# Kernel optimization log

Measured on AMD Instinct MI355X. Metric: run time of the kernel, lower is better.

## Reference

```python
import jax, jax.numpy as jnp
import numpy as np

N_BUS = 200000; N_GEN = 50000
E_BB = 1600000; E_GB = 400000; E_BG = 400000
D_IN = 64; H = 32
OUT_BUS = 4; OUT_GEN = 2


def setup_inputs() -> dict:
    key = jax.random.key(0)
    it = iter(jax.random.split(key, 48))
    def nrm(shape, s=0.05):
        return jax.random.normal(next(it), shape, jnp.float32) * s
    inp = {}
    inp["x_bus"] = jax.random.normal(next(it), (N_BUS, D_IN), jnp.float32)
    inp["x_gen"] = jax.random.normal(next(it), (N_GEN, D_IN), jnp.float32)
    inp["src_bb"] = jax.random.randint(next(it), (E_BB,), 0, N_BUS)
    inp["dst_bb"] = jax.random.randint(next(it), (E_BB,), 0, N_BUS)
    inp["src_gb"] = jax.random.randint(next(it), (E_GB,), 0, N_GEN)
    inp["dst_gb"] = jax.random.randint(next(it), (E_GB,), 0, N_BUS)
    inp["src_bg"] = jax.random.randint(next(it), (E_BG,), 0, N_BUS)
    inp["dst_bg"] = jax.random.randint(next(it), (E_BG,), 0, N_GEN)
    # SAGEConv params per layer / relation: lin_l (on aggregated neighbors, with bias),
    # lin_r (root weight on x_dst, no bias) -- matches PyG SAGEConv defaults.
    for lname, din in (("l1", D_IN), ("l2", H)):
        for rel in ("bb", "gb", "bg"):
            inp[f"{lname}_{rel}_Wl"] = nrm((din, H))
            inp[f"{lname}_{rel}_bl"] = jnp.zeros((H,), jnp.float32)
            inp[f"{lname}_{rel}_Wr"] = nrm((din, H))
    for nt, dout in (("bus", OUT_BUS), ("gen", OUT_GEN)):
        inp[f"lin0_{nt}_W"] = nrm((H, H))
        inp[f"lin0_{nt}_b"] = jnp.zeros((H,), jnp.float32)
        inp[f"linf_{nt}_W"] = nrm((H, dout))
        inp[f"linf_{nt}_b"] = jnp.zeros((dout,), jnp.float32)
    return inp


def _sage(x_src, x_dst, src, dst, Wl, bl, Wr, n_dst):
    # SAGEConv: mean-aggregate neighbor features, then out = lin_l(mean) + lin_r(x_dst)
    msg = jax.ops.segment_sum(x_src[src], dst, num_segments=n_dst)
    cnt = jax.ops.segment_sum(jnp.ones((src.shape[0],), x_src.dtype), dst, num_segments=n_dst)
    mean = msg / jnp.maximum(cnt, 1.0)[:, None]
    return mean @ Wl + bl + x_dst @ Wr


def reference(x_bus, x_gen, src_bb, dst_bb, src_gb, dst_gb, src_bg, dst_bg,
              l1_bb_Wl, l1_bb_bl, l1_bb_Wr, l1_gb_Wl, l1_gb_bl, l1_gb_Wr,
              l1_bg_Wl, l1_bg_bl, l1_bg_Wr,
              l2_bb_Wl, l2_bb_bl, l2_bb_Wr, l2_gb_Wl, l2_gb_bl, l2_gb_Wr,
              l2_bg_Wl, l2_bg_bl, l2_bg_Wr,
              lin0_bus_W, lin0_bus_b, lin0_gen_W, lin0_gen_b,
              linf_bus_W, linf_bus_b, linf_gen_W, linf_gen_b):
    # HeteroConv layer 1 (aggr='sum' over relations targeting each dst type)
    hb = (_sage(x_bus, x_bus, src_bb, dst_bb, l1_bb_Wl, l1_bb_bl, l1_bb_Wr, N_BUS)
          + _sage(x_gen, x_bus, src_gb, dst_gb, l1_gb_Wl, l1_gb_bl, l1_gb_Wr, N_BUS))
    hg = _sage(x_bus, x_gen, src_bg, dst_bg, l1_bg_Wl, l1_bg_bl, l1_bg_Wr, N_GEN)
    xb, xg = jax.nn.relu(hb), jax.nn.relu(hg)  # dropout is identity in eval mode
    # HeteroConv layer 2
    hb = (_sage(xb, xb, src_bb, dst_bb, l2_bb_Wl, l2_bb_bl, l2_bb_Wr, N_BUS)
          + _sage(xg, xb, src_gb, dst_gb, l2_gb_Wl, l2_gb_bl, l2_gb_Wr, N_BUS))
    hg = _sage(xb, xg, src_bg, dst_bg, l2_bg_Wl, l2_bg_bl, l2_bg_Wr, N_GEN)
    xb, xg = jax.nn.relu(hb), jax.nn.relu(hg)
    # per-node-type hidden Linear (input relu'd again as in the original; relu is idempotent)
    xb = jax.nn.relu(xb) @ lin0_bus_W + lin0_bus_b
    xg = jax.nn.relu(xg) @ lin0_gen_W + lin0_gen_b
    out_bus = xb @ linf_bus_W + linf_bus_b
    out_gen = xg @ linf_gen_W + linf_gen_b
    return out_bus, out_gen
```

## Files before the change

kernel.cpp:

```cpp
#include <hip/hip_runtime.h>
#include <hip/hip_bf16.h>

#define N_BUS 200000
#define N_GEN 50000
#define E_BB 1600000
#define E_GB 400000
#define E_BG 400000
#define H 32
#define NBINS 1024
#define EPT 16

#define NBK_BUS 782
#define NBK_GEN 196
#define CAP_BB 2560
#define CAP_GB 768
#define CAP_BG 2560

#define NB_PART_BB 391
#define NB_PART_GB 98
#define NB_PART_BG 98
#define NB_PART_ALL 587
#define NB_PREP 32
#define NB_TF_BUS 782
#define NB_TF_GEN 196
#define NB_TF_ALL 978
#define NB_FINE_ALL 1760
#define NB_PL_BUS 6250
#define NB_PL_GEN 1563

#define PNONE 0xFFFFFFFFu

typedef __attribute__((ext_vector_type(8))) short short8;
typedef __attribute__((ext_vector_type(4))) float floatx4;

__device__ inline unsigned short f2bf(float f) {
    __hip_bfloat16 h = __float2bfloat16(f);
    return *reinterpret_cast<unsigned short*>(&h);
}
__device__ inline float bf2f(unsigned short u) {
    return __uint_as_float(((unsigned)u) << 16);
}

__global__ __launch_bounds__(256) void zero_kernel(unsigned* __restrict__ p) {
    int i = blockIdx.x * 256 + threadIdx.x;
    if (i < 3 * NBINS) p[i] = 0u;
}

__device__ __forceinline__ void part_body(int blk, const int* __restrict__ src,
                                          const int* __restrict__ dst, int nE,
                                          unsigned* __restrict__ cnt_g, int CAP,
                                          unsigned* __restrict__ pairs) {
    __shared__ unsigned hist[NBINS];
    __shared__ unsigned base[NBINS];
    __shared__ unsigned sbase[NBINS];
    __shared__ unsigned sh[256];
    __shared__ unsigned pairv[256 * EPT];
    __shared__ unsigned short bid[256 * EPT];
    const int tid = threadIdx.x;
    const int cbase = blk * (256 * EPT);
    const int total = min(256 * EPT, nE - cbase);

    unsigned es[EPT], ed[EPT];
#pragma unroll
    for (int q = 0; q < EPT; q++) {
        int i = cbase + q * 256 + tid;
        if (i < nE) { es[q] = (unsigned)src[i]; ed[q] = (unsigned)dst[i]; }
        else ed[q] = PNONE;
    }
    for (int i = tid; i < NBINS; i += 256) hist[i] = 0;
    __syncthreads();
#pragma unroll
    for (int q = 0; q < EPT; q++)
        if (ed[q] != PNONE) atomicAdd(&hist[ed[q] >> 8], 1u);
    __syncthreads();

    unsigned h4[4];
    unsigned s = 0;
#pragma unroll
    for (int k2 = 0; k2 < 4; k2++) { h4[k2] = hist[tid * 4 + k2]; s += h4[k2]; }
    sh[tid] = s;
    __syncthreads();
#pragma unroll
    for (int d = 1; d < 256; d <<= 1) {
        unsigned t = (tid >= d) ? sh[tid - d] : 0u;
        __syncthreads();
        sh[tid] += t;
        __syncthreads();
    }
    unsigned run = sh[tid] - s;
#pragma unroll
    for (int k2 = 0; k2 < 4; k2++) {
        int b = tid * 4 + k2;
        sbase[b] = run;
        base[b] = h4[k2] ? ((unsigned)b * CAP + atomicAdd(&cnt_g[b], h4[k2])) : 0u;
        hist[b] = 0;
        run += h4[k2];
    }
    __syncthreads();

#pragma unroll
    for (int q = 0; q < EPT; q++) {
        if (ed[q] != PNONE) {
            unsigned b = ed[q] >> 8;
            unsigned off = atomicAdd(&hist[b], 1u);
            unsigned p = sbase[b] + off;
            pairv[p] = ((ed[q] & 255u) << 24) | es[q];
            bid[p] = (unsigned short)b;
        }
    }
    __syncthreads();

    for (int p = tid; p < total; p += 256) {
        unsigned b = bid[p];
        pairs[base[b] + ((unsigned)p - sbase[b])] = pairv[p];
    }
}

__device__ __forceinline__ void prep_body(int pb,
    const float* __restrict__ l1_bb_Wl, const float* __restrict__ l1_bb_bl, const float* __restrict__ l1_bb_Wr,
    const float* __restrict__ l1_gb_Wl, const float* __restrict__ l1_gb_bl, const float* __restrict__ l1_gb_Wr,
    const float* __restrict__ l1_bg_Wl, const float* __restrict__ l1_bg_bl, const float* __restrict__ l1_bg_Wr,
    const float* __restrict__ l2_bb_Wl, const float* __restrict__ l2_bb_bl, const float* __restrict__ l2_bb_Wr,
    const float* __restrict__ l2_gb_Wl, const float* __restrict__ l2_gb_bl, const float* __restrict__ l2_gb_Wr,
    const float* __restrict__ l2_bg_Wl, const float* __restrict__ l2_bg_bl, const float* __restrict__ l2_bg_Wr,
    const float* __restrict__ lin0_bus_W, const float* __restrict__ lin0_bus_b,
    const float* __restrict__ linf_bus_W, const float* __restrict__ linf_bus_b,
    const float* __restrict__ lin0_gen_W, const float* __restrict__ lin0_gen_b,
    const float* __restrict__ linf_gen_W, const float* __restrict__ linf_gen_b,
    unsigned short* __restrict__ Wf1b, float* __restrict__ B1b,
    unsigned short* __restrict__ Wf1g, float* __restrict__ B1g,
    unsigned short* __restrict__ Wf2b, float* __restrict__ B2b,
    unsigned short* __restrict__ Wf2g, float* __restrict__ B2g,
    float* __restrict__ WeB, float* __restrict__ beB,
    float* __restrict__ WeG, float* __restrict__ beG)
{
    int t0 = pb * 256 + threadIdx.x;
    const int NT = NB_PREP * 256;

    for (int f = t0; f < 2 * 6 * 64 * 8; f += NT) {
        int j = f & 7, l = (f >> 3) & 63, tile = f >> 9;
        int nt = tile % 6, kt = tile / 6;
        int k = kt * 32 + (l >> 4) * 8 + j, n = nt * 16 + (l & 15);
        float v;
        if (n < 32) v = l1_bb_Wl[k * 32 + n];
        else if (n < 64) v = l1_bg_Wl[k * 32 + n - 32];
        else v = l1_bb_Wr[k * 32 + n - 64] + l1_gb_Wr[k * 32 + n - 64];
        Wf1b[f] = f2bf(v);
    }
    for (int f = t0; f < 2 * 4 * 64 * 8; f += NT) {
        int j = f & 7, l = (f >> 3) & 63, tile = f >> 9;
        int nt = tile % 4, kt = tile / 4;
        int k = kt * 32 + (l >> 4) * 8 + j, n = nt * 16 + (l & 15);
        float v = (n < 32) ? l1_gb_Wl[k * 32 + n] : l1_bg_Wr[k * 32 + n - 32];
        Wf1g[f] = f2bf(v);
    }
    for (int f = t0; f < 6 * 64 * 8; f += NT) {
        int j = f & 7, l = (f >> 3) & 63, nt = f >> 9;
        int k = (l >> 4) * 8 + j, n = nt * 16 + (l & 15);
        float v;
        if (n < 32) v = l2_bb_Wl[k * 32 + n];
        else if (n < 64) v = l2_bg_Wl[k * 32 + n - 32];
        else v = l2_bb_Wr[k * 32 + n - 64] + l2_gb_Wr[k * 32 + n - 64];
        Wf2b[f] = f2bf(v);
    }
    for (int f = t0; f < 4 * 64 * 8; f += NT) {
        int j = f & 7, l = (f >> 3) & 63, nt = f >> 9;
        int k = (l >> 4) * 8 + j, n = nt * 16 + (l & 15);
        float v = (n < 32) ? l2_gb_Wl[k * 32 + n] : l2_bg_Wr[k * 32 + n - 32];
        Wf2g[f] = f2bf(v);
    }
    if (t0 < 96) {
        B1b[t0] = (t0 < 64) ? 0.0f : l1_bb_bl[t0 - 64] + l1_gb_bl[t0 - 64];
        B2b[t0] = (t0 < 64) ? 0.0f : l2_bb_bl[t0 - 64] + l2_gb_bl[t0 - 64];
    }
    if (t0 < 64) {
        B1g[t0] = (t0 < 32) ? 0.0f : l1_bg_bl[t0 - 32];
        B2g[t0] = (t0 < 32) ? 0.0f : l2_bg_bl[t0 - 32];
    }
    if (t0 < 128) {
        int k = t0 >> 2, c = t0 & 3;
        float s = 0.0f;
        for (int m = 0; m < 32; m++) s += lin0_bus_W[k * 32 + m] * linf_bus_W[m * 4 + c];
        WeB[t0] = s;
    }
    if (t0 >= 128 && t0 < 132) {
        int c = t0 - 128;
        float s = linf_bus_b[c];
        for (int m = 0; m < 32; m++) s += lin0_bus_b[m] * linf_bus_W[m * 4 + c];
        beB[c] = s;
    }
    if (t0 >= 132 && t0 < 196) {
        int i = t0 - 132, k = i >> 1, c = i & 1;
        float s = 0.0f;
        for (int m = 0; m < 32; m++) s += lin0_gen_W[k * 32 + m] * linf_gen_W[m * 2 + c];
        WeG[i] = s;
    }
    if (t0 >= 196 && t0 < 198) {
        int c = t0 - 196;
        float s = linf_gen_b[c];
        for (int m = 0; m < 32; m++) s += lin0_gen_b[m] * linf_gen_W[m * 2 + c];
        beG[c] = s;
    }
}

__global__ __launch_bounds__(256) void prep_part_kernel(
    const int* __restrict__ sbb, const int* __restrict__ dbb, unsigned* __restrict__ cbb, unsigned* __restrict__ pbb,
    const int* __restrict__ sgb, const int* __restrict__ dgb, unsigned* __restrict__ cgb, unsigned* __restrict__ pgb,
    const int* __restrict__ sbg, const int* __restrict__ dbg, unsigned* __restrict__ cbg, unsigned* __restrict__ pbg,
    const float* __restrict__ l1_bb_Wl, const float* __restrict__ l1_bb_bl, const float* __restrict__ l1_bb_Wr,
    const float* __restrict__ l1_gb_Wl, const float* __restrict__ l1_gb_bl, const float* __restrict__ l1_gb_Wr,
    const float* __restrict__ l1_bg_Wl, const float* __restrict__ l1_bg_bl, const float* __restrict__ l1_bg_Wr,
    const float* __restrict__ l2_bb_Wl, const float* __restrict__ l2_bb_bl, const float* __restrict__ l2_bb_Wr,
    const float* __restrict__ l2_gb_Wl, const float* __restrict__ l2_gb_bl, const float* __restrict__ l2_gb_Wr,
    const float* __restrict__ l2_bg_Wl, const float* __restrict__ l2_bg_bl, const float* __restrict__ l2_bg_Wr,
    const float* __restrict__ lin0_bus_W, const float* __restrict__ lin0_bus_b,
    const float* __restrict__ linf_bus_W, const float* __restrict__ linf_bus_b,
    const float* __restrict__ lin0_gen_W, const float* __restrict__ lin0_gen_b,
    const float* __restrict__ linf_gen_W, const float* __restrict__ linf_gen_b,
    unsigned short* __restrict__ Wf1b, float* __restrict__ B1b,
    unsigned short* __restrict__ Wf1g, float* __restrict__ B1g,
    unsigned short* __restrict__ Wf2b, float* __restrict__ B2b,
    unsigned short* __restrict__ Wf2g, float* __restrict__ B2g,
    float* __restrict__ WeB, float* __restrict__ beB,
    float* __restrict__ WeG, float* __restrict__ beG)
{
    int b = blockIdx.x;
    if (b < NB_PART_BB) part_body(b, sbb, dbb, E_BB, cbb, CAP_BB, pbb);
    else if (b < NB_PART_BB + NB_PART_GB) part_body(b - NB_PART_BB, sgb, dgb, E_GB, cgb, CAP_GB, pgb);
    else if (b < NB_PART_ALL) part_body(b - NB_PART_BB - NB_PART_GB, sbg, dbg, E_BG, cbg, CAP_BG, pbg);
    else prep_body(b - NB_PART_ALL,
                   l1_bb_Wl, l1_bb_bl, l1_bb_Wr, l1_gb_Wl, l1_gb_bl, l1_gb_Wr,
                   l1_bg_Wl, l1_bg_bl, l1_bg_Wr, l2_bb_Wl, l2_bb_bl, l2_bb_Wr,
                   l2_gb_Wl, l2_gb_bl, l2_gb_Wr, l2_bg_Wl, l2_bg_bl, l2_bg_Wr,
                   lin0_bus_W, lin0_bus_b, linf_bus_W, linf_bus_b,
                   lin0_gen_W, lin0_gen_b, linf_gen_W, linf_gen_b,
                   Wf1b, B1b, Wf1g, B1g, Wf2b, B2b, Wf2g, B2g, WeB, beB, WeG, beG);
}

__device__ __forceinline__ void fine_body(int b, const unsigned* __restrict__ cnt_g, int CAP,
                                          const unsigned* __restrict__ pairs,
                                          unsigned* __restrict__ rs,
                                          unsigned* __restrict__ esrc, int nDst,
                                          char* __restrict__ lds) {
    unsigned* cnt = (unsigned*)lds;
    unsigned* sh = (unsigned*)(lds + 1024);
    unsigned* stg = (unsigned*)(lds + 2048);
    const int tid = threadIdx.x;
    const unsigned start = (unsigned)b * CAP;
    const unsigned m = cnt_g[b];
    const unsigned end = start + m;

    cnt[tid] = 0;
    __syncthreads();
    for (unsigned k = start + tid; k < end; k += 256)
        atomicAdd(&cnt[pairs[k] >> 24], 1u);
    __syncthreads();
    unsigned c = cnt[tid];
    sh[tid] = c;
    __syncthreads();
#pragma unroll
    for (int d = 1; d < 256; d <<= 1) {
        unsigned t = (tid >= d) ? sh[tid - d] : 0u;
        __syncthreads();
        sh[tid] += t;
        __syncthreads();
    }
    int gd = b * 256 + tid;
    unsigned rowstart = start + sh[tid] - c;
    if (gd < nDst) rs[gd] = (rowstart << 9) | (c < 511u ? c : 511u);
    cnt[tid] = sh[tid] - c;
    __syncthreads();
    for (unsigned k = start + tid; k < end; k += 256) {
        unsigned p = pairs[k];
        unsigned off = atomicAdd(&cnt[p >> 24], 1u);
        stg[off] = p & 0x00FFFFFFu;
    }
    __syncthreads();
    for (unsigned p = tid; p < m; p += 256) esrc[start + p] = stg[p];
}

template <int K, int NOUT, int XS>
__device__ __forceinline__ void mfma_tail(
    int rows, int base,
    const unsigned short* __restrict__ Wf, const float* __restrict__ bias,
    unsigned short* __restrict__ y0, unsigned short* __restrict__ y1, float* __restrict__ h,
    short* lx, float* lo)
{
    constexpr int KT = K / 32, NTN = NOUT / 16, NCH = NOUT / 32;
    constexpr int OS = 34;
    const int tid = threadIdx.x;
    const int w = tid >> 6, l = tid & 63, quad = l >> 4, ln = l & 15;

    short8 bf[KT][NTN];
    const short8* wf8 = (const short8*)Wf;
#pragma unroll
    for (int kt = 0; kt < KT; kt++)
#pragma unroll
        for (int nt = 0; nt < NTN; nt++)
            bf[kt][nt] = wf8[(kt * NTN + nt) * 64 + l];
    float bv[NTN];
#pragma unroll
    for (int nt = 0; nt < NTN; nt++) bv[nt] = bias[nt * 16 + ln];

    floatx4 acc[4][NTN];
#pragma unroll
    for (int mt = 0; mt < 4; mt++)
#pragma unroll
        for (int nt = 0; nt < NTN; nt++) {
            floatx4 c0 = {bv[nt], bv[nt], bv[nt], bv[nt]};
            acc[mt][nt] = c0;
        }
#pragma unroll
    for (int mt = 0; mt < 4; mt++) {
        const int row = w * 64 + mt * 16 + ln;
#pragma unroll
        for (int kt = 0; kt < KT; kt++) {
            short8 af = *(const short8*)&lx[row * XS + kt * 32 + quad * 8];
#pragma unroll
            for (int nt = 0; nt < NTN; nt++)
                acc[mt][nt] = __builtin_amdgcn_mfma_f32_16x16x32_bf16(
                    af, bf[kt][nt], acc[mt][nt], 0, 0, 0);
        }
    }

#pragma unroll
    for (int c = 0; c < NCH; c++) {
        __syncthreads();
#pragma unroll
        for (int mt = 0; mt < 4; mt++)
#pragma unroll
            for (int d = 0; d < 2; d++) {
                int nt = 2 * c + d;
#pragma unroll
                for (int r = 0; r < 4; r++)
                    lo[(w * 64 + mt * 16 + quad * 4 + r) * OS + d * 16 + ln] = acc[mt][nt][r];
            }
        __syncthreads();
        const int T4 = rows * 8;
        if (c == NCH - 1) {
            float* og = h + (size_t)base * 32;
            for (int q = tid; q < T4; q += 256) {
                int r = q >> 3, cc = (q & 7) * 4;
                const float* p = &lo[r * OS + cc];
                *(float4*)(og + q * 4) = make_float4(p[0], p[1], p[2], p[3]);
            }
        } else {
            unsigned short* og = ((c == 0) ? y0 : y1) + (size_t)base * 32;
            for (int q = tid; q < T4; q += 256) {
                int r = q >> 3, cc = (q & 7) * 4;
                const float* p = &lo[r * OS + cc];
                short4 s4;
                s4.x = (short)f2bf(p[0]); s4.y = (short)f2bf(p[1]);
                s4.z = (short)f2bf(p[2]); s4.w = (short)f2bf(p[3]);
                *(short4*)(og + q * 4) = s4;
            }
        }
    }
}

template <int K, int NOUT>
__device__ __forceinline__ void transform_body(
    int blk, const float* x, int n,
    const unsigned short* __restrict__ Wf, const float* __restrict__ bias,
    unsigned short* __restrict__ y0, unsigned short* __restrict__ y1, float* h,
    char* ldsraw)
{
    constexpr int XS = K + 8;
    short* lx = (short*)ldsraw;
    const int tid = threadIdx.x;
    const int base = blk * 256;
    const int rows = min(256, n - base);

    {
        const float4* xg = (const float4*)(x + (size_t)base * K);
        const int T4 = rows * (K / 4);
        for (int q = tid; q < T4; q += 256) {
            float4 v = xg[q];
            int r = q / (K / 4), c = (q % (K / 4)) * 4;
            short4 s4;
            s4.x = (short)f2bf(v.x); s4.y = (short)f2bf(v.y);
            s4.z = (short)f2bf(v.z); s4.w = (short)f2bf(v.w);
            *(short4*)&lx[r * XS + c] = s4;
        }
    }
    __syncthreads();
    mfma_tail<K, NOUT, XS>(rows, base, Wf, bias, y0, y1, h, (short*)ldsraw, (float*)ldsraw);
}

__global__ __launch_bounds__(256) void tf1_fine_kernel(
    const float* xb, const unsigned short* __restrict__ Wfb, const float* __restrict__ Bb,
    unsigned short* __restrict__ yb0, unsigned short* __restrict__ yb1, float* hb,
    const float* xg, const unsigned short* __restrict__ Wfg, const float* __restrict__ Bg,
    unsigned short* __restrict__ yg0, float* hg,
    const unsigned* __restrict__ cbb, const unsigned* __restrict__ pbb, unsigned* __restrict__ rsbb, unsigned* __restrict__ ebb,
    const unsigned* __restrict__ cgb, const unsigned* __restrict__ pgb, unsigned* __restrict__ rsgb, unsigned* __restrict__ egb,
    const unsigned* __restrict__ cbg, const unsigned* __restrict__ pbg, unsigned* __restrict__ rsbg, unsigned* __restrict__ ebg)
{
    constexpr int XB = 256 * (64 + 8) * 2, OB = 256 * 34 * 4;
    __shared__ __align__(16) char ldsraw[(XB > OB) ? XB : OB];
    int b = blockIdx.x;
    if (b < NB_TF_BUS)
        transform_body<64, 96>(b, xb, N_BUS, Wfb, Bb, yb0, yb1, hb, ldsraw);
    else if (b < NB_TF_ALL)
        transform_body<64, 64>(b - NB_TF_BUS, xg, N_GEN, Wfg, Bg, yg0, nullptr, hg, ldsraw);
    else {
        int f = b - NB_TF_ALL;
        if (f < NBK_BUS) fine_body(f, cbb, CAP_BB, pbb, rsbb, ebb, N_BUS, ldsraw);
        else if (f < 2 * NBK_BUS) fine_body(f - NBK_BUS, cgb, CAP_GB, pgb, rsgb, egb, N_BUS, ldsraw);
        else fine_body(f - 2 * NBK_BUS, cbg, CAP_BG, pbg, rsbg, ebg, N_GEN, ldsraw);
    }
}

__device__ __forceinline__ void agg_one(
    unsigned u, const unsigned* __restrict__ e,
    const unsigned short* __restrict__ y, int j, float4& r)
{
    unsigned k0 = u >> 9;
    unsigned c = u & 511u;
    unsigned k1 = k0 + c;
    float4 a0 = make_float4(0.f, 0.f, 0.f, 0.f);
    float4 a1 = a0, a2 = a0, a3 = a0;
    unsigned k = k0;
    if (k + 4 <= k1) {
        unsigned s0 = e[k], s1 = e[k + 1], s2 = e[k + 2], s3 = e[k + 3];
        for (; k + 8 <= k1; k += 4) {
            unsigned t0 = e[k + 4], t1 = e[k + 5], t2 = e[k + 6], t3 = e[k + 7];
            ushort4 v0 = *(const ushort4*)(y + (size_t)s0 * H + j);
            ushort4 v1 = *(const ushort4*)(y + (size_t)s1 * H + j);
            ushort4 v2 = *(const ushort4*)(y + (size_t)s2 * H + j);
            ushort4 v3 = *(const ushort4*)(y + (size_t)s3 * H + j);
            a0.x += bf2f(v0.x); a0.y += bf2f(v0.y); a0.z += bf2f(v0.z); a0.w += bf2f(v0.w);
            a1.x += bf2f(v1.x); a1.y += bf2f(v1.y); a1.z += bf2f(v1.z); a1.w += bf2f(v1.w);
            a2.x += bf2f(v2.x); a2.y += bf2f(v2.y); a2.z += bf2f(v2.z); a2.w += bf2f(v2.w);
            a3.x += bf2f(v3.x); a3.y += bf2f(v3.y); a3.z += bf2f(v3.z); a3.w += bf2f(v3.w);
            s0 = t0; s1 = t1; s2 = t2; s3 = t3;
        }
        {
            ushort4 v0 = *(const ushort4*)(y + (size_t)s0 * H + j);
            ushort4 v1 = *(const ushort4*)(y + (size_t)s1 * H + j);
            ushort4 v2 = *(const ushort4*)(y + (size_t)s2 * H + j);
            ushort4 v3 = *(const ushort4*)(y + (size_t)s3 * H + j);
            a0.x += bf2f(v0.x); a0.y += bf2f(v0.y); a0.z += bf2f(v0.z); a0.w += bf2f(v0.w);
            a1.x += bf2f(v1.x); a1.y += bf2f(v1.y); a1.z += bf2f(v1.z); a1.w += bf2f(v1.w);
            a2.x += bf2f(v2.x); a2.y += bf2f(v2.y); a2.z += bf2f(v2.z); a2.w += bf2f(v2.w);
            a3.x += bf2f(v3.x); a3.y += bf2f(v3.y); a3.z += bf2f(v3.z); a3.w += bf2f(v3.w);
            k += 4;
        }
    }
    for (; k < k1; ++k) {
        unsigned s = e[k];
        const ushort4 v = *(const ushort4*)(y + (size_t)s * H + j);
        a0.x += bf2f(v.x); a0.y += bf2f(v.y); a0.z += bf2f(v.z); a0.w += bf2f(v.w);
    }
    a0.x += a1.x + a2.x + a3.x; a0.y += a1.y + a2.y + a3.y;
    a0.z += a1.z + a2.z + a3.z; a0.w += a1.w + a2.w + a3.w;
    float inv = 1.0f / (float)(c > 1u ? c : 1u);
    r.x += a0.x * inv; r.y += a0.y * inv; r.z += a0.z * inv; r.w += a0.w * inv;
}

template <int NTA, bool HASB>
__device__ __forceinline__ void pull_tf_body(
    int blk, int n,
    const unsigned* __restrict__ rsA, const unsigned* __restrict__ eA, const unsigned short* __restrict__ yA,
    const unsigned* __restrict__ rsB, const unsigned* __restrict__ eB, const unsigned short* __restrict__ yB,
    float* __restrict__ h,
    const unsigned short* __restrict__ Wf, const float* __restrict__ bias,
    unsigned short* __restrict__ z0, unsigned short* __restrict__ z1,
    short* __restrict__ lx, float* __restrict__ lo)
{
    constexpr int XS = 40;
    constexpr int OS = 34;
    const int tid = threadIdx.x;
    const int row = tid >> 3;
    const int j = (tid & 7) * 4;
    const int base = blk * 32;
    const int node = base + row;
    const bool act = node < n;

    float4 r = make_float4(0.f, 0.f, 0.f, 0.f);
    if (act) {
        r = *(const float4*)(h + (size_t)node * H + j);
        agg_one(rsA[node], eA, yA, j, r);
        if (HASB) agg_one(rsB[node], eB, yB, j, r);
    }
    short4 s4;
    s4.x = (short)f2bf(fmaxf(r.x, 0.f));
    s4.y = (short)f2bf(fmaxf(r.y, 0.f));
    s4.z = (short)f2bf(fmaxf(r.z, 0.f));
    s4.w = (short)f2bf(fmaxf(r.w, 0.f));
    *(short4*)&lx[row * XS + j] = s4;
    __syncthreads();

    const int w = tid >> 6, l = tid & 63, quad = l >> 4, ln = l & 15;
    const int mt = w & 1, ngrp = w >> 1;
    const short8* wf8 = (const short8*)Wf;
    floatx4 acc[NTA];
    short8 af = *(const short8*)&lx[(mt * 16 + ln) * XS + quad * 8];
#pragma unroll
    for (int i = 0; i < NTA; i++) {
        int nt = 2 * i + ngrp;
        float bv = bias[nt * 16 + ln];
        floatx4 c0 = {bv, bv, bv, bv};
        acc[i] = __builtin_amdgcn_mfma_f32_16x16x32_bf16(af, wf8[nt * 64 + l], c0, 0, 0, 0);
    }

    const int rows = min(32, n - base);
    const int orow = tid >> 3, oc = (tid & 7) * 4;
#pragma unroll
    for (int c = 0; c < NTA; c++) {
        __syncthreads();
#pragma unroll
        for (int rr = 0; rr < 4; rr++)
            lo[(mt * 16 + quad * 4 + rr) * OS + ngrp * 16 + ln] = acc[c][rr];
        __syncthreads();
        if (orow < rows) {
            const float* p = &lo[orow * OS + oc];
            if (c == NTA - 1) {
                *(float4*)(h + (size_t)(base + orow) * H + oc) =
                    make_float4(p[0], p[1], p[2], p[3]);
            } else {
                unsigned short* og = (c == 0) ? z0 : z1;
                short4 o;
                o.x = (short)f2bf(p[0]); o.y = (short)f2bf(p[1]);
                o.z = (short)f2bf(p[2]); o.w = (short)f2bf(p[3]);
                *(short4*)(og + (size_t)(base + orow) * H + oc) = o;
            }
        }
    }
}

__global__ __launch_bounds__(256) void pull_tf2_kernel(
    const unsigned* __restrict__ rsbb, const unsigned* __restrict__ ebb, const unsigned short* __restrict__ ybb,
    const unsigned* __restrict__ rsgb, const unsigned* __restrict__ egb, const unsigned short* __restrict__ ygb,
    float* __restrict__ hb, const unsigned short* __restrict__ Wfb, const float* __restrict__ Bb,
    unsigned short* __restrict__ y2bb, unsigned short* __restrict__ y2bg,
    const unsigned* __restrict__ rsbg, const unsigned* __restrict__ ebg, const unsigned short* __restrict__ ybg,
    float* __restrict__ hg, const unsigned short* __restrict__ Wfg, const float* __restrict__ Bg,
    unsigned short* __restrict__ y2gb)
{
    __shared__ __align__(16) short lx[32 * 40];
    __shared__ __align__(16) float lo[32 * 34];
    int b = blockIdx.x;
    if (b < NB_PL_BUS)
        pull_tf_body<3, true>(b, N_BUS, rsbb, ebb, ybb, rsgb, egb, ygb,
                              hb, Wfb, Bb, y2bb, y2bg, lx, lo);
    else
        pull_tf_body<2, false>(b - NB_PL_BUS, N_GEN, rsbg, ebg, ybg,
                               nullptr, nullptr, nullptr,
                               hg, Wfg, Bg, y2gb, nullptr, lx, lo);
}

__device__ __forceinline__ void pull_head_body(
    int blk, bool hasB, int n,
    const unsigned* __restrict__ rsA, const unsigned* __restrict__ eA, const unsigned short* __restrict__ yA,
    const unsigned* __restrict__ rsB, const unsigned* __restrict__ eB, const unsigned short* __restrict__ yB,
    const float* __restrict__ h,
    const float* __restrict__ We, const float* __restrict__ be, int DOUT, float* __restrict__ outp)
{
    const int tid = threadIdx.x;
    unsigned node = blk * 32u + (tid >> 3);
    int j = (tid & 7) * 4;
    if (node >= (unsigned)n) return;

    float4 r = *(const float4*)(h + (size_t)node * H + j);

    agg_one(rsA[node], eA, yA, j, r);
    if (hasB) agg_one(rsB[node], eB, yB, j, r);

    float p0 = fmaxf(r.x, 0.f), p1 = fmaxf(r.y, 0.f), p2 = fmaxf(r.z, 0.f), p3 = fmaxf(r.w, 0.f);
    float tot[4];
#pragma unroll
    for (int c = 0; c < 4; c++) {
        if (c < DOUT) {
            tot[c] = p0 * We[(j + 0) * DOUT + c] + p1 * We[(j + 1) * DOUT + c]
                   + p2 * We[(j + 2) * DOUT + c] + p3 * We[(j + 3) * DOUT + c];
        } else tot[c] = 0.f;
    }
#pragma unroll
    for (int mask = 1; mask <= 4; mask <<= 1) {
#pragma unroll
        for (int c = 0; c < 4; c++) tot[c] += __shfl_xor(tot[c], mask);
    }
    if ((tid & 7) == 0) {
        if (DOUT == 4) {
            *(float4*)(outp + (size_t)node * 4) =
                make_float4(tot[0] + be[0], tot[1] + be[1], tot[2] + be[2], tot[3] + be[3]);
        } else {
            *(float2*)(outp + (size_t)node * 2) = make_float2(tot[0] + be[0], tot[1] + be[1]);
        }
    }
}

__global__ __launch_bounds__(256) void pull_head_kernel(
    const unsigned* __restrict__ rsbb, const unsigned* __restrict__ ebb, const unsigned short* __restrict__ y2bb,
    const unsigned* __restrict__ rsgb, const unsigned* __restrict__ egb, const unsigned short* __restrict__ y2gb,
    const float* __restrict__ hb, const float* __restrict__ WeB, const float* __restrict__ beB,
    const unsigned* __restrict__ rsbg, const unsigned* __restrict__ ebg, const unsigned short* __restrict__ y2bg,
    const float* __restrict__ hg, const float* __restrict__ WeG, const float* __restrict__ beG,
    float* __restrict__ outp)
{
    int b = blockIdx.x;
    if (b < NB_PL_BUS)
        pull_head_body(b, true, N_BUS, rsbb, ebb, y2bb, rsgb, egb, y2gb, hb, WeB, beB, 4, outp);
    else
        pull_head_body(b - NB_PL_BUS, false, N_GEN, rsbg, ebg, y2bg, nullptr, nullptr, nullptr,
                       hg, WeG, beG, 2, outp + (size_t)N_BUS * 4);
}

extern "C" void kernel_launch(void* const* d_in, const int* in_sizes, int n_in,
                              void* d_out, int out_size, void* d_ws, size_t ws_size,
                              hipStream_t stream) {
    const float* x_bus = (const float*)d_in[0];
    const float* x_gen = (const float*)d_in[1];
    const int* src_bb = (const int*)d_in[2];
    const int* dst_bb = (const int*)d_in[3];
    const int* src_gb = (const int*)d_in[4];
    const int* dst_gb = (const int*)d_in[5];
    const int* src_bg = (const int*)d_in[6];
    const int* dst_bg = (const int*)d_in[7];
    const float* l1_bb_Wl = (const float*)d_in[8];
    const float* l1_bb_bl = (const float*)d_in[9];
    const float* l1_bb_Wr = (const float*)d_in[10];
    const float* l1_gb_Wl = (const float*)d_in[11];
    const float* l1_gb_bl = (const float*)d_in[12];
    const float* l1_gb_Wr = (const float*)d_in[13];
    const float* l1_bg_Wl = (const float*)d_in[14];
    const float* l1_bg_bl = (const float*)d_in[15];
    const float* l1_bg_Wr = (const float*)d_in[16];
    const float* l2_bb_Wl = (const float*)d_in[17];
    const float* l2_bb_bl = (const float*)d_in[18];
    const float* l2_bb_Wr = (const float*)d_in[19];
    const float* l2_gb_Wl = (const float*)d_in[20];
    const float* l2_gb_bl = (const float*)d_in[21];
    const float* l2_gb_Wr = (const float*)d_in[22];
    const float* l2_bg_Wl = (const float*)d_in[23];
    const float* l2_bg_bl = (const float*)d_in[24];
    const float* l2_bg_Wr = (const float*)d_in[25];
    const float* lin0_bus_W = (const float*)d_in[26];
    const float* lin0_bus_b = (const float*)d_in[27];
    const float* linf_bus_W = (const float*)d_in[28];
    const float* linf_bus_b = (const float*)d_in[29];
    const float* lin0_gen_W = (const float*)d_in[30];
    const float* lin0_gen_b = (const float*)d_in[31];
    const float* linf_gen_W = (const float*)d_in[32];
    const float* linf_gen_b = (const float*)d_in[33];

    char* ws = (char*)d_ws;
    size_t off = 0;
    auto alloc = [&](size_t bytes) {
        char* p = ws + off;
        off += (bytes + 255) & ~(size_t)255;
        return p;
    };
    unsigned* rs_bb = (unsigned*)alloc((size_t)N_BUS * 4);
    unsigned* rs_gb = (unsigned*)alloc((size_t)N_BUS * 4);
    unsigned* rs_bg = (unsigned*)alloc((size_t)N_GEN * 4);
    unsigned* cur_bb = (unsigned*)alloc(NBINS * 4);
    unsigned* cur_gb = (unsigned*)alloc(NBINS * 4);
    unsigned* cur_bg = (unsigned*)alloc(NBINS * 4);
    unsigned* e_bb = (unsigned*)alloc((size_t)NBK_BUS * CAP_BB * 4);
    unsigned* e_gb = (unsigned*)alloc((size_t)NBK_BUS * CAP_GB * 4);
    unsigned* e_bg = (unsigned*)alloc((size_t)NBK_GEN * CAP_BG * 4);
    unsigned* p_bb = (unsigned*)alloc((size_t)NBK_BUS * CAP_BB * 4);
    unsigned* p_gb = (unsigned*)alloc((size_t)NBK_BUS * CAP_GB * 4);
    unsigned* p_bg = (unsigned*)alloc((size_t)NBK_GEN * CAP_BG * 4);
    unsigned short* y_bb = (unsigned short*)alloc((size_t)N_BUS * H * 2);
    unsigned short* y_bg = (unsigned short*)alloc((size_t)N_BUS * H * 2);
    unsigned short* y_gb = (unsigned short*)alloc((size_t)N_GEN * H * 2);
    unsigned short* y2_bb = (unsigned short*)alloc((size_t)N_BUS * H * 2);
    unsigned short* y2_bg = (unsigned short*)alloc((size_t)N_BUS * H * 2);
    unsigned short* y2_gb = (unsigned short*)alloc((size_t)N_GEN * H * 2);
    float* h_bus = (float*)alloc((size_t)N_BUS * H * 4);
    float* h_gen = (float*)alloc((size_t)N_GEN * H * 4);
    unsigned short* Wf1b = (unsigned short*)alloc(2 * 6 * 64 * 8 * 2);
    float* B1b = (float*)alloc(96 * 4);
    unsigned short* Wf1g = (unsigned short*)alloc(2 * 4 * 64 * 8 * 2);
    float* B1g = (float*)alloc(64 * 4);
    unsigned short* Wf2b = (unsigned short*)alloc(6 * 64 * 8 * 2);
    float* B2b = (float*)alloc(96 * 4);
    unsigned short* Wf2g = (unsigned short*)alloc(4 * 64 * 8 * 2);
    float* B2g = (float*)alloc(64 * 4);
    float* WeB = (float*)alloc(128 * 4);
    float* beB = (float*)alloc(4 * 4);
    float* WeG = (float*)alloc(64 * 4);
    float* beG = (float*)alloc(2 * 4);

    zero_kernel<<<12, 256, 0, stream>>>(cur_bb);

    prep_part_kernel<<<NB_PART_ALL + NB_PREP, 256, 0, stream>>>(
        src_bb, dst_bb, cur_bb, p_bb, src_gb, dst_gb, cur_gb, p_gb,
        src_bg, dst_bg, cur_bg, p_bg,
        l1_bb_Wl, l1_bb_bl, l1_bb_Wr, l1_gb_Wl, l1_gb_bl, l1_gb_Wr,
        l1_bg_Wl, l1_bg_bl, l1_bg_Wr, l2_bb_Wl, l2_bb_bl, l2_bb_Wr,
        l2_gb_Wl, l2_gb_bl, l2_gb_Wr, l2_bg_Wl, l2_bg_bl, l2_bg_Wr,
        lin0_bus_W, lin0_bus_b, linf_bus_W, linf_bus_b,
        lin0_gen_W, lin0_gen_b, linf_gen_W, linf_gen_b,
        Wf1b, B1b, Wf1g, B1g, Wf2b, B2b, Wf2g, B2g, WeB, beB, WeG, beG);

    tf1_fine_kernel<<<NB_TF_ALL + NB_FINE_ALL, 256, 0, stream>>>(
        x_bus, Wf1b, B1b, y_bb, y_bg, h_bus, x_gen, Wf1g, B1g, y_gb, h_gen,
        cur_bb, p_bb, rs_bb, e_bb, cur_gb, p_gb, rs_gb, e_gb, cur_bg, p_bg, rs_bg, e_bg);

    pull_tf2_kernel<<<NB_PL_BUS + NB_PL_GEN, 256, 0, stream>>>(
        rs_bb, e_bb, y_bb, rs_gb, e_gb, y_gb, h_bus, Wf2b, B2b, y2_bb, y2_bg,
        rs_bg, e_bg, y_bg, h_gen, Wf2g, B2g, y2_gb);

    pull_head_kernel<<<NB_PL_BUS + NB_PL_GEN, 256, 0, stream>>>(
        rs_bb, e_bb, y2_bb, rs_gb, e_gb, y2_gb, h_bus, WeB, beB,
        rs_bg, e_bg, y2_bg, h_gen, WeG, beG, (float*)d_out);
}
```

Before: 359.2 us.

## Use wave-shuffle block scans, smaller transform tiles, and single-pass output staging

Swaps the LDS Hillis-Steele scans in the partition and fine-bucketing bodies for a warp-shuffle scan with per-wave sums, which cuts many barriers. The layer-1 transform now handles 128 rows per block instead of 256, doubling block count and shrinking LDS. It also reads weight fragments directly inside the MFMA loop instead of holding them in registers. The pull-transform epilogue stages all output chunks into a wider LDS buffer at once, trading several barrier rounds for more LDS use per block.

```diff
diff --git a/kernel.cpp b/kernel.cpp
--- a/kernel.cpp
+++ b/kernel.cpp
@@ -21,9 +21,9 @@
 #define NB_PART_BG 98
 #define NB_PART_ALL 587
 #define NB_PREP 32
-#define NB_TF_BUS 782
-#define NB_TF_GEN 196
-#define NB_TF_ALL 978
+#define NB_TF1_BUS 1563
+#define NB_TF1_GEN 391
+#define NB_TF1_ALL 1954
 #define NB_FINE_ALL 1760
 #define NB_PL_BUS 6250
 #define NB_PL_GEN 1563
@@ -39,6 +39,21 @@
 }
 __device__ inline float bf2f(unsigned short u) {
     return __uint_as_float(((unsigned)u) << 16);
+}
+
+__device__ __forceinline__ unsigned block_excl_scan(unsigned s, unsigned* wsum) {
+    const int lane = threadIdx.x & 63, wv = threadIdx.x >> 6;
+    unsigned scan = s;
+#pragma unroll
+    for (int d = 1; d < 64; d <<= 1) {
+        unsigned t = __shfl_up(scan, d, 64);
+        if (lane >= d) scan += t;
+    }
+    if (lane == 63) wsum[wv] = scan;
+    __syncthreads();
+    unsigned base = 0;
+    for (int i = 0; i < wv; i++) base += wsum[i];
+    return base + scan - s;
 }
 
 __global__ __launch_bounds__(256) void zero_kernel(unsigned* __restrict__ p) {
@@ -53,7 +68,7 @@
     __shared__ unsigned hist[NBINS];
     __shared__ unsigned base[NBINS];
     __shared__ unsigned sbase[NBINS];
-    __shared__ unsigned sh[256];
+    __shared__ unsigned wsum[4];
     __shared__ unsigned pairv[256 * EPT];
     __shared__ unsigned short bid[256 * EPT];
     const int tid = threadIdx.x;
@@ -78,16 +93,7 @@
     unsigned s = 0;
 #pragma unroll
     for (int k2 = 0; k2 < 4; k2++) { h4[k2] = hist[tid * 4 + k2]; s += h4[k2]; }
-    sh[tid] = s;
-    __syncthreads();
-#pragma unroll
-    for (int d = 1; d < 256; d <<= 1) {
-        unsigned t = (tid >= d) ? sh[tid - d] : 0u;
-        __syncthreads();
-        sh[tid] += t;
-        __syncthreads();
-    }
-    unsigned run = sh[tid] - s;
+    unsigned run = block_excl_scan(s, wsum);
 #pragma unroll
     for (int k2 = 0; k2 < 4; k2++) {
         int b = tid * 4 + k2;
@@ -243,7 +249,7 @@
                                           unsigned* __restrict__ esrc, int nDst,
                                           char* __restrict__ lds) {
     unsigned* cnt = (unsigned*)lds;
-    unsigned* sh = (unsigned*)(lds + 1024);
+    unsigned* wsum = (unsigned*)(lds + 1024);
     unsigned* stg = (unsigned*)(lds + 2048);
     const int tid = threadIdx.x;
     const unsigned start = (unsigned)b * CAP;
@@ -256,19 +262,11 @@
         atomicAdd(&cnt[pairs[k] >> 24], 1u);
     __syncthreads();
     unsigned c = cnt[tid];
-    sh[tid] = c;
-    __syncthreads();
-#pragma unroll
-    for (int d = 1; d < 256; d <<= 1) {
-        unsigned t = (tid >= d) ? sh[tid - d] : 0u;
-        __syncthreads();
-        sh[tid] += t;
-        __syncthreads();
-    }
+    unsigned excl = block_excl_scan(c, wsum);
     int gd = b * 256 + tid;
-    unsigned rowstart = start + sh[tid] - c;
+    unsigned rowstart = start + excl;
     if (gd < nDst) rs[gd] = (rowstart << 9) | (c < 511u ? c : 511u);
-    cnt[tid] = sh[tid] - c;
+    cnt[tid] = excl;
     __syncthreads();
     for (unsigned k = start + tid; k < end; k += 256) {
         unsigned p = pairs[k];
@@ -279,47 +277,61 @@
     for (unsigned p = tid; p < m; p += 256) esrc[start + p] = stg[p];
 }
 
-template <int K, int NOUT, int XS>
-__device__ __forceinline__ void mfma_tail(
-    int rows, int base,
+template <int K, int NOUT, int ROWS>
+__device__ __forceinline__ void transform_body(
+    int blk, const float* x, int n,
     const unsigned short* __restrict__ Wf, const float* __restrict__ bias,
-    unsigned short* __restrict__ y0, unsigned short* __restrict__ y1, float* __restrict__ h,
-    short* lx, float* lo)
-{
+    unsigned short* __restrict__ y0, unsigned short* __restrict__ y1, float* h,
+    char* ldsraw)
+{
+    constexpr int XS = K + 8;
     constexpr int KT = K / 32, NTN = NOUT / 16, NCH = NOUT / 32;
+    constexpr int MTW = ROWS / 64;
     constexpr int OS = 34;
+    short* lx = (short*)ldsraw;
+    float* lo = (float*)ldsraw;
     const int tid = threadIdx.x;
+    const int base = blk * ROWS;
+    const int rows = min(ROWS, n - base);
     const int w = tid >> 6, l = tid & 63, quad = l >> 4, ln = l & 15;
 
-    short8 bf[KT][NTN];
+    {
+        const float4* xg = (const float4*)(x + (size_t)base * K);
+        const int T4 = rows * (K / 4);
+        for (int q = tid; q < T4; q += 256) {
+            float4 v = xg[q];
+            int r = q / (K / 4), c = (q % (K / 4)) * 4;
+            short4 s4;
+            s4.x = (short)f2bf(v.x); s4.y = (short)f2bf(v.y);
+            s4.z = (short)f2bf(v.z); s4.w = (short)f2bf(v.w);
+            *(short4*)&lx[r * XS + c] = s4;
+        }
+    }
+    __syncthreads();
+
     const short8* wf8 = (const short8*)Wf;
-#pragma unroll
-    for (int kt = 0; kt < KT; kt++)
-#pragma unroll
-        for (int nt = 0; nt < NTN; nt++)
-            bf[kt][nt] = wf8[(kt * NTN + nt) * 64 + l];
     float bv[NTN];
 #pragma unroll
     for (int nt = 0; nt < NTN; nt++) bv[nt] = bias[nt * 16 + ln];
 
-    floatx4 acc[4][NTN];
-#pragma unroll
-    for (int mt = 0; mt < 4; mt++)
+    floatx4 acc[MTW][NTN];
+#pragma unroll
+    for (int mt = 0; mt < MTW; mt++)
 #pragma unroll
         for (int nt = 0; nt < NTN; nt++) {
             floatx4 c0 = {bv[nt], bv[nt], bv[nt], bv[nt]};
             acc[mt][nt] = c0;
         }
 #pragma unroll
-    for (int mt = 0; mt < 4; mt++) {
-        const int row = w * 64 + mt * 16 + ln;
+    for (int mt = 0; mt < MTW; mt++) {
+        const int row = w * (ROWS / 4) + mt * 16 + ln;
 #pragma unroll
         for (int kt = 0; kt < KT; kt++) {
             short8 af = *(const short8*)&lx[row * XS + kt * 32 + quad * 8];
 #pragma unroll
             for (int nt = 0; nt < NTN; nt++)
                 acc[mt][nt] = __builtin_amdgcn_mfma_f32_16x16x32_bf16(
-                    af, bf[kt][nt], acc[mt][nt], 0, 0, 0);
+                    af, wf8[(kt * NTN + nt) * 64 + l], acc[mt][nt], 0, 0, 0);
         }
     }
 
@@ -327,13 +339,13 @@
     for (int c = 0; c < NCH; c++) {
         __syncthreads();
 #pragma unroll
-        for (int mt = 0; mt < 4; mt++)
+        for (int mt = 0; mt < MTW; mt++)
 #pragma unroll
             for (int d = 0; d < 2; d++) {
                 int nt = 2 * c + d;
 #pragma unroll
                 for (int r = 0; r < 4; r++)
-                    lo[(w * 64 + mt * 16 + quad * 4 + r) * OS + d * 16 + ln] = acc[mt][nt][r];
+                    lo[(w * (ROWS / 4) + mt * 16 + quad * 4 + r) * OS + d * 16 + ln] = acc[mt][nt][r];
             }
         __syncthreads();
         const int T4 = rows * 8;
@@ -358,35 +370,6 @@
     }
 }
 
-template <int K, int NOUT>
-__device__ __forceinline__ void transform_body(
-    int blk, const float* x, int n,
-    const unsigned short* __restrict__ Wf, const float* __restrict__ bias,
-    unsigned short* __restrict__ y0, unsigned short* __restrict__ y1, float* h,
-    char* ldsraw)
-{
-    constexpr int XS = K + 8;
-    short* lx = (short*)ldsraw;
-    const int tid = threadIdx.x;
-    const int base = blk * 256;
-    const int rows = min(256, n - base);
-
-    {
-        const float4* xg = (const float4*)(x + (size_t)base * K);
-        const int T4 = rows * (K / 4);
-        for (int q = tid; q < T4; q += 256) {
-            float4 v = xg[q];
-            int r = q / (K / 4), c = (q % (K / 4)) * 4;
-            short4 s4;
-            s4.x = (short)f2bf(v.x); s4.y = (short)f2bf(v.y);
-            s4.z = (short)f2bf(v.z); s4.w = (short)f2bf(v.w);
-            *(short4*)&lx[r * XS + c] = s4;
-        }
-    }
-    __syncthreads();
-    mfma_tail<K, NOUT, XS>(rows, base, Wf, bias, y0, y1, h, (short*)ldsraw, (float*)ldsraw);
-}
-
 __global__ __launch_bounds__(256) void tf1_fine_kernel(
     const float* xb, const unsigned short* __restrict__ Wfb, const float* __restrict__ Bb,
     unsigned short* __restrict__ yb0, unsigned short* __restrict__ yb1, float* hb,
@@ -396,15 +379,15 @@
     const unsigned* __restrict__ cgb, const unsigned* __restrict__ pgb, unsigned* __restrict__ rsgb, unsigned* __restrict__ egb,
     const unsigned* __restrict__ cbg, const unsigned* __restrict__ pbg, unsigned* __restrict__ rsbg, unsigned* __restrict__ ebg)
 {
-    constexpr int XB = 256 * (64 + 8) * 2, OB = 256 * 34 * 4;
+    constexpr int XB = 128 * (64 + 8) * 2, OB = 128 * 34 * 4;
     __shared__ __align__(16) char ldsraw[(XB > OB) ? XB : OB];
     int b = blockIdx.x;
-    if (b < NB_TF_BUS)
-        transform_body<64, 96>(b, xb, N_BUS, Wfb, Bb, yb0, yb1, hb, ldsraw);
-    else if (b < NB_TF_ALL)
-        transform_body<64, 64>(b - NB_TF_BUS, xg, N_GEN, Wfg, Bg, yg0, nullptr, hg, ldsraw);
+    if (b < NB_TF1_BUS)
+        transform_body<64, 96, 128>(b, xb, N_BUS, Wfb, Bb, yb0, yb1, hb, ldsraw);
+    else if (b < NB_TF1_ALL)
+        transform_body<64, 64, 128>(b - NB_TF1_BUS, xg, N_GEN, Wfg, Bg, yg0, nullptr, hg, ldsraw);
     else {
-        int f = b - NB_TF_ALL;
+        int f = b - NB_TF1_ALL;
         if (f < NBK_BUS) fine_body(f, cbb, CAP_BB, pbb, rsbb, ebb, N_BUS, ldsraw);
         else if (f < 2 * NBK_BUS) fine_body(f - NBK_BUS, cgb, CAP_GB, pgb, rsgb, egb, N_BUS, ldsraw);
         else fine_body(f - 2 * NBK_BUS, cbg, CAP_BG, pbg, rsbg, ebg, N_GEN, ldsraw);
@@ -469,7 +452,7 @@
     short* __restrict__ lx, float* __restrict__ lo)
 {
     constexpr int XS = 40;
-    constexpr int OS = 34;
+    constexpr int OS2 = NTA * 32 + 4;
     const int tid = threadIdx.x;
     const int row = tid >> 3;
     const int j = (tid & 7) * 4;
@@ -504,26 +487,32 @@
         acc[i] = __builtin_amdgcn_mfma_f32_16x16x32_bf16(af, wf8[nt * 64 + l], c0, 0, 0, 0);
     }
 
+#pragma unroll
+    for (int i = 0; i < NTA; i++) {
+        int colb = (2 * i + ngrp) * 16 + ln;
+#pragma unroll
+        for (int rr = 0; rr < 4; rr++)
+            lo[(mt * 16 + quad * 4 + rr) * OS2 + colb] = acc[i][rr];
+    }
+    __syncthreads();
     const int rows = min(32, n - base);
-    const int orow = tid >> 3, oc = (tid & 7) * 4;
-#pragma unroll
-    for (int c = 0; c < NTA; c++) {
-        __syncthreads();
-#pragma unroll
-        for (int rr = 0; rr < 4; rr++)
-            lo[(mt * 16 + quad * 4 + rr) * OS + ngrp * 16 + ln] = acc[c][rr];
-        __syncthreads();
+    constexpr int NC4 = NTA * 8;
+#pragma unroll
+    for (int t = 0; t < NTA; t++) {
+        int q = tid + t * 256;
+        int orow = q / NC4, c4 = (q % NC4) * 4;
         if (orow < rows) {
-            const float* p = &lo[orow * OS + oc];
-            if (c == NTA - 1) {
-                *(float4*)(h + (size_t)(base + orow) * H + oc) =
+            const float* p = &lo[orow * OS2 + c4];
+            int chunk = c4 >> 5;
+            if (chunk == NTA - 1) {
+                *(float4*)(h + (size_t)(base + orow) * H + (c4 & 31)) =
                     make_float4(p[0], p[1], p[2], p[3]);
             } else {
-                unsigned short* og = (c == 0) ? z0 : z1;
+                unsigned short* og = (chunk == 0) ? z0 : z1;
                 short4 o;
                 o.x = (short)f2bf(p[0]); o.y = (short)f2bf(p[1]);
                 o.z = (short)f2bf(p[2]); o.w = (short)f2bf(p[3]);
-                *(short4*)(og + (size_t)(base + orow) * H + oc) = o;
+                *(short4*)(og + (size_t)(base + orow) * H + (c4 & 31)) = o;
             }
         }
     }
@@ -539,7 +528,7 @@
     unsigned short* __restrict__ y2gb)
 {
     __shared__ __align__(16) short lx[32 * 40];
-    __shared__ __align__(16) float lo[32 * 34];
+    __shared__ __align__(16) float lo[32 * 100];
     int b = blockIdx.x;
     if (b < NB_PL_BUS)
         pull_tf_body<3, true>(b, N_BUS, rsbb, ebb, ybb, rsgb, egb, ygb,
@@ -697,7 +686,7 @@
         lin0_gen_W, lin0_gen_b, linf_gen_W, linf_gen_b,
         Wf1b, B1b, Wf1g, B1g, Wf2b, B2b, Wf2g, B2g, WeB, beB, WeG, beG);
 
-    tf1_fine_kernel<<<NB_TF_ALL + NB_FINE_ALL, 256, 0, stream>>>(
+    tf1_fine_kernel<<<NB_TF1_ALL + NB_FINE_ALL, 256, 0, stream>>>(
         x_bus, Wf1b, B1b, y_bb, y_bg, h_bus, x_gen, Wf1g, B1g, y_gb, h_gen,
         cur_bb, p_bb, rs_bb, e_bb, cur_gb, p_gb, rs_gb, e_gb, cur_bg, p_bg, rs_bg, e_bg);
 
```

New measurement: 350.0 us. 2.6% less time.
